# Optimization experiments

Measured on AMD Instinct MI355X. Metric: run time of the kernel, lower is better.

Reference implementation:

```python
import jax, jax.numpy as jnp
import numpy as np

N = 50000      # nodes
E = 800000     # edges (avg degree 16)
IN = 128       # input feature dim
H = 128        # hidden dim (all layers output H; out_channels unused in source)
DROP_P = 0.5


def setup_inputs() -> dict:
    key = jax.random.key(0)
    ks = jax.random.split(key, 8)
    s_in = 1.0 / np.sqrt(IN).astype(np.float32)
    s_h = 1.0 / np.sqrt(H).astype(np.float32)
    return {
        "x": jax.random.normal(ks[0], (N, IN), jnp.float32),
        "edge_index": jax.random.randint(ks[1], (2, E), 0, N, dtype=jnp.int32),
        "Wl0": jax.random.normal(ks[2], (H, IN), jnp.float32) * s_in,
        "bl0": jnp.zeros((H,), jnp.float32),
        "Wr0": jax.random.normal(ks[3], (H, IN), jnp.float32) * s_in,
        "Wl1": jax.random.normal(ks[4], (H, H), jnp.float32) * s_h,
        "bl1": jnp.zeros((H,), jnp.float32),
        "Wr1": jax.random.normal(ks[5], (H, H), jnp.float32) * s_h,
    }


def _sage_conv(x, src, dst, Wl, bl, Wr):
    # mean-aggregate neighbor messages: gather x[src], scatter-add to dst
    agg = jax.ops.segment_sum(x[src], dst, num_segments=N)          # [N, D]
    deg = jax.ops.segment_sum(jnp.ones((src.shape[0],), x.dtype), dst,
                              num_segments=N)                        # [N]
    agg = agg / jnp.maximum(deg, 1.0)[:, None]                       # scatter_mean (0 for isolated nodes)
    # PyG SAGEConv: lin_l(agg) (with bias) + lin_r(x) (no bias)
    return agg @ Wl.T + bl + x @ Wr.T


def reference(x, edge_index, Wl0, bl0, Wr0, Wl1, bl1, Wr1):
    src, dst = edge_index[0], edge_index[1]
    h = _sage_conv(x, src, dst, Wl0, bl0, Wr0)
    h = jax.nn.relu(h)
    # dropout(p=0.5, training=True) with a fixed key for determinism
    keep = jax.random.bernoulli(jax.random.key(42), 1.0 - DROP_P, h.shape)
    h = jnp.where(keep, h / (1.0 - DROP_P), 0.0)
    out = _sage_conv(h, src, dst, Wl1, bl1, Wr1)
    return out
```

## Files before the change

### kernel.cpp

```cpp
#include <hip/hip_runtime.h>
#include <hip/hip_bf16.h>


#define HDIM 128
#define KDIM 256
#define NBUK 256
#define BNODE 196
#define BCH 2048

typedef __attribute__((ext_vector_type(8))) short bshort8;
typedef __attribute__((ext_vector_type(4))) float f32x4;

__device__ __forceinline__ ushort f2b(float f) {
  __hip_bfloat16 h = __float2bfloat16(f);
  return *(ushort*)&h;
}
__device__ __forceinline__ float blo(unsigned int v) { return __uint_as_float(v << 16); }
__device__ __forceinline__ float bhi(unsigned int v) { return __uint_as_float(v & 0xffff0000u); }

__device__ __forceinline__ unsigned int tf_rotl(unsigned int x, int d) {
  return (x << d) | (x >> (32 - d));
}
__device__ __forceinline__ bool dropout_keep(unsigned int j) {
  unsigned int x0 = 0u, x1 = j;
  const unsigned int ks0 = 0u, ks1 = 42u, ks2 = 0x1BD11BDAu ^ 0u ^ 42u;
  x0 += ks0; x1 += ks1;
#define TF_R(r) { x0 += x1; x1 = tf_rotl(x1, (r)); x1 ^= x0; }
  TF_R(13) TF_R(15) TF_R(26) TF_R(6)
  x0 += ks1; x1 += ks2 + 1u;
  TF_R(17) TF_R(29) TF_R(16) TF_R(24)
  x0 += ks2; x1 += ks0 + 2u;
  TF_R(13) TF_R(15) TF_R(26) TF_R(6)
  x0 += ks0; x1 += ks1 + 3u;
  TF_R(17) TF_R(29) TF_R(16) TF_R(24)
  x0 += ks1; x1 += ks2 + 4u;
  TF_R(13) TF_R(15) TF_R(26) TF_R(6)
  x0 += ks2; x1 += ks0 + 5u;
#undef TF_R
  unsigned int r = x0 ^ x1;
  float u = __uint_as_float((r >> 9) | 0x3f800000u) - 1.0f;
  return u < 0.5f;
}

__global__ __launch_bounds__(256) void bhist_k(const int* __restrict__ dst,
                                               int* __restrict__ bucketCount, int E) {
  __shared__ int h[NBUK];
  h[threadIdx.x] = 0;
  __syncthreads();
  int begin = blockIdx.x * BCH;
  int n = min(BCH, E - begin);
  for (int i = threadIdx.x; i < n; i += 256) atomicAdd(&h[dst[begin + i] / BNODE], 1);
  __syncthreads();
  if (h[threadIdx.x]) atomicAdd(&bucketCount[threadIdx.x], h[threadIdx.x]);
}

__global__ __launch_bounds__(256) void bscan_k(const int* __restrict__ bucketCount,
                                               int* __restrict__ bucketStart,
                                               int* __restrict__ cursor) {
  __shared__ int tmp[NBUK];
  int v = bucketCount[threadIdx.x];
  tmp[threadIdx.x] = v;
  __syncthreads();
  for (int off = 1; off < NBUK; off <<= 1) {
    int t = (threadIdx.x >= off) ? tmp[threadIdx.x - off] : 0;
    __syncthreads();
    tmp[threadIdx.x] += t;
    __syncthreads();
  }
  int ex = tmp[threadIdx.x] - v;
  bucketStart[threadIdx.x] = ex;
  cursor[threadIdx.x] = ex;
}

__global__ __launch_bounds__(256) void bin_k(const int* __restrict__ src,
                                             const int* __restrict__ dst,
                                             int* __restrict__ cursor,
                                             unsigned int* __restrict__ pairs, int E) {
  __shared__ int hist[NBUK];
  __shared__ int lofs[NBUK];
  __shared__ int lcur[NBUK];
  __shared__ int gbase[NBUK];
  __shared__ unsigned int ordv[BCH];
  __shared__ unsigned char ordb[BCH];
  hist[threadIdx.x] = 0;
  __syncthreads();
  int begin = blockIdx.x * BCH;
  int n = min(BCH, E - begin);
  unsigned int vals[BCH / 256];
  int bks[BCH / 256];
  int cnt = 0;
  for (int i = threadIdx.x; i < n; i += 256) {
    int s = src[begin + i], d = dst[begin + i];
    int b = d / BNODE;
    int dloc = d - b * BNODE;
    vals[cnt] = ((unsigned int)s << 8) | (unsigned int)dloc;
    bks[cnt] = b;
    ++cnt;
    atomicAdd(&hist[b], 1);
  }
  __syncthreads();
  {
    int v = hist[threadIdx.x];
    lofs[threadIdx.x] = v;
    __syncthreads();
    for (int off = 1; off < NBUK; off <<= 1) {
      int t = (threadIdx.x >= off) ? lofs[threadIdx.x - off] : 0;
      __syncthreads();
      lofs[threadIdx.x] += t;
      __syncthreads();
    }
    int ex = lofs[threadIdx.x] - v;
    __syncthreads();
    lofs[threadIdx.x] = ex;
    lcur[threadIdx.x] = ex;
    gbase[threadIdx.x] = atomicAdd(&cursor[threadIdx.x], v);
  }
  __syncthreads();
  for (int k = 0; k < cnt; ++k) {
    int b = bks[k];
    int p = atomicAdd(&lcur[b], 1);
    ordv[p] = vals[k];
    ordb[p] = (unsigned char)b;
  }
  __syncthreads();
  for (int j = threadIdx.x; j < n; j += 256) {
    int b = ordb[j];
    pairs[gbase[b] + (j - lofs[b])] = ordv[j];
  }
}

__global__ __launch_bounds__(256) void build_k(const unsigned int* __restrict__ pairs,
                                               const int* __restrict__ bucketStart,
                                               const int* __restrict__ bucketCount,
                                               int* __restrict__ deg,
                                               int* __restrict__ rowptr,
                                               ushort* __restrict__ eidx, int N) {
  __shared__ int h[BNODE];
  __shared__ int lofs[BNODE];
  __shared__ int cur[BNODE];
  const int b = blockIdx.x;
  const int base = bucketStart[b];
  const int cnt = bucketCount[b];
  const int nodebase = b * BNODE;
  const int nloc = min(BNODE, N - nodebase);
  if (threadIdx.x < BNODE) h[threadIdx.x] = 0;
  __syncthreads();
  for (int i = threadIdx.x; i < cnt; i += 256) atomicAdd(&h[pairs[base + i] & 255u], 1);
  __syncthreads();
  if (threadIdx.x < BNODE) lofs[threadIdx.x] = h[threadIdx.x];
  __syncthreads();
  for (int off = 1; off < BNODE; off <<= 1) {
    int t = (threadIdx.x >= off && threadIdx.x < BNODE) ? lofs[threadIdx.x - off] : 0;
    __syncthreads();
    if (threadIdx.x < BNODE) lofs[threadIdx.x] += t;
    __syncthreads();
  }
  if (threadIdx.x < BNODE) {
    int ex = lofs[threadIdx.x] - h[threadIdx.x];
    cur[threadIdx.x] = ex;
    if (threadIdx.x < nloc) {
      deg[nodebase + threadIdx.x] = h[threadIdx.x];
      rowptr[nodebase + threadIdx.x] = base + ex;
    }
  }
  __syncthreads();
  for (int i = threadIdx.x; i < cnt; i += 256) {
    unsigned int v = pairs[base + i];
    int pos = atomicAdd(&cur[v & 255u], 1);
    eidx[base + pos] = (ushort)(v >> 8);
  }
}

__global__ __launch_bounds__(256) void cvt_x_k(const float* __restrict__ x,
                                               ushort* __restrict__ Ab, int N) {
  int t = blockIdx.x * 256 + threadIdx.x;
  if (t >= N * 32) return;
  int n = t >> 5, c4 = t & 31;
  float4 v = *(const float4*)&x[(size_t)n * HDIM + c4 * 4];
  uint2 p;
  p.x = (unsigned int)f2b(v.x) | ((unsigned int)f2b(v.y) << 16);
  p.y = (unsigned int)f2b(v.z) | ((unsigned int)f2b(v.w) << 16);
  *(uint2*)&Ab[(size_t)n * KDIM + HDIM + c4 * 4] = p;
}

__global__ __launch_bounds__(256) void cvt_w_k(const float* __restrict__ Wl0,
                                               const float* __restrict__ Wr0,
                                               const float* __restrict__ Wl1,
                                               const float* __restrict__ Wr1,
                                               ushort* __restrict__ Wc0,
                                               ushort* __restrict__ Wc1) {
  int t = blockIdx.x * 256 + threadIdx.x;
  int o = t >> 7, k = t & 127;
  Wc0[o * KDIM + k] = f2b(Wl0[t]);
  Wc0[o * KDIM + HDIM + k] = f2b(Wr0[t]);
  Wc1[o * KDIM + k] = f2b(Wl1[t]);
  Wc1[o * KDIM + HDIM + k] = f2b(Wr1[t]);
}

__global__ __launch_bounds__(256) void agg_b(const ushort* __restrict__ Xb,
                                             ushort* __restrict__ Ob,
                                             const ushort* __restrict__ eidx,
                                             const int* __restrict__ rowptr,
                                             const int* __restrict__ deg, int N) {
  const int lane = threadIdx.x & 63;
  const int n = blockIdx.x * 4 + (threadIdx.x >> 6);
  if (n >= N) return;
  const int start = rowptr[n];
  const int d = deg[n];
  const int co = 2 * lane;
  float a0 = 0.0f, a1 = 0.0f;
  int j = 0;
  for (; j + 4 <= d; j += 4) {
    int s0 = eidx[start + j + 0];
    int s1 = eidx[start + j + 1];
    int s2 = eidx[start + j + 2];
    int s3 = eidx[start + j + 3];
    unsigned int v0 = *(const unsigned int*)&Xb[(size_t)s0 * KDIM + HDIM + co];
    unsigned int v1 = *(const unsigned int*)&Xb[(size_t)s1 * KDIM + HDIM + co];
    unsigned int v2 = *(const unsigned int*)&Xb[(size_t)s2 * KDIM + HDIM + co];
    unsigned int v3 = *(const unsigned int*)&Xb[(size_t)s3 * KDIM + HDIM + co];
    a0 += blo(v0) + blo(v1) + blo(v2) + blo(v3);
    a1 += bhi(v0) + bhi(v1) + bhi(v2) + bhi(v3);
  }
  for (; j < d; ++j) {
    int s = eidx[start + j];
    unsigned int v = *(const unsigned int*)&Xb[(size_t)s * KDIM + HDIM + co];
    a0 += blo(v);
    a1 += bhi(v);
  }
  float rd = 1.0f / fmaxf((float)d, 1.0f);
  unsigned int p = (unsigned int)f2b(a0 * rd) | ((unsigned int)f2b(a1 * rd) << 16);
  *(unsigned int*)&Ob[(size_t)n * KDIM + co] = p;
}

template <int MODE>
__global__ __launch_bounds__(256) void gemm_mfma(const ushort* __restrict__ A,
                                                 const ushort* __restrict__ Wc,
                                                 ushort* __restrict__ hb,
                                                 float* __restrict__ fout,
                                                 const float* __restrict__ bias,
                                                 int N) {
  __shared__ char smem[67584];
  ushort* Wl = (ushort*)smem;
  float* Tl = (float*)smem;
  const int tid = threadIdx.x;
  const int lane = tid & 63;
  const int wid = tid >> 6;
  const int quad = lane >> 4;
  const int l15 = lane & 15;
  const int n0 = blockIdx.x * 64;

#pragma unroll
  for (int i = 0; i < 16; ++i) {
    int q = i * 256 + tid;
    int row = q >> 5, seg = q & 31;
    *(uint4*)&Wl[row * 264 + seg * 8] = *(const uint4*)&Wc[row * KDIM + seg * 8];
  }

  int rowA = n0 + wid * 16 + l15;
  if (rowA >= N) rowA = N - 1;
  bshort8 af[8];
#pragma unroll
  for (int ks = 0; ks < 8; ++ks)
    af[ks] = *(const bshort8*)&A[(size_t)rowA * KDIM + ks * 32 + quad * 8];

  f32x4 acc[8];
#pragma unroll
  for (int i = 0; i < 8; ++i) acc[i] = (f32x4){0.f, 0.f, 0.f, 0.f};

  __syncthreads();

#pragma unroll
  for (int ks = 0; ks < 8; ++ks) {
#pragma unroll
    for (int os = 0; os < 8; ++os) {
      bshort8 bf = *(const bshort8*)&Wl[(os * 16 + l15) * 264 + ks * 32 + quad * 8];
      acc[os] = __builtin_amdgcn_mfma_f32_16x16x32_bf16(af[ks], bf, acc[os], 0, 0, 0);
    }
  }

  __syncthreads();

  const int wbase = wid * (16 * 132);
#pragma unroll
  for (int os = 0; os < 8; ++os)
#pragma unroll
    for (int r = 0; r < 4; ++r)
      Tl[wbase + (quad * 4 + r) * 132 + os * 16 + l15] = acc[os][r];

  __syncthreads();

#pragma unroll
  for (int i = 0; i < 8; ++i) {
    int q = i * 64 + lane;
    int r = q >> 5;
    int c4 = q & 31;
    int n = n0 + wid * 16 + r;
    if (n >= N) continue;
    int c = c4 * 4;
    float4 v = *(float4*)&Tl[wbase + r * 132 + c];
    const float4 bv = *(const float4*)&bias[c];
    v.x += bv.x; v.y += bv.y; v.z += bv.z; v.w += bv.w;
    if (MODE == 1) {
      v.x = v.x > 0.0f ? v.x : 0.0f;
      v.y = v.y > 0.0f ? v.y : 0.0f;
      v.z = v.z > 0.0f ? v.z : 0.0f;
      v.w = v.w > 0.0f ? v.w : 0.0f;
      unsigned int fj = (unsigned int)n * HDIM + (unsigned int)c;
      v.x = dropout_keep(fj + 0u) ? v.x * 2.0f : 0.0f;
      v.y = dropout_keep(fj + 1u) ? v.y * 2.0f : 0.0f;
      v.z = dropout_keep(fj + 2u) ? v.z * 2.0f : 0.0f;
      v.w = dropout_keep(fj + 3u) ? v.w * 2.0f : 0.0f;
      uint2 p;
      p.x = (unsigned int)f2b(v.x) | ((unsigned int)f2b(v.y) << 16);
      p.y = (unsigned int)f2b(v.z) | ((unsigned int)f2b(v.w) << 16);
      *(uint2*)&hb[(size_t)n * KDIM + HDIM + c] = p;
    } else {
      *(float4*)&fout[(size_t)n * HDIM + c] = v;
    }
  }
}

extern "C" void kernel_launch(void* const* d_in, const int* in_sizes, int n_in,
                              void* d_out, int out_size, void* d_ws, size_t ws_size,
                              hipStream_t stream) {
  const float* x   = (const float*)d_in[0];
  const int*   ei  = (const int*)d_in[1];
  const float* Wl0 = (const float*)d_in[2];
  const float* bl0 = (const float*)d_in[3];
  const float* Wr0 = (const float*)d_in[4];
  const float* Wl1 = (const float*)d_in[5];
  const float* bl1 = (const float*)d_in[6];
  const float* Wr1 = (const float*)d_in[7];
  float* out = (float*)d_out;

  const int N = in_sizes[0] / HDIM;
  const int E = in_sizes[1] / 2;
  const int* src = ei;
  const int* dst = ei + E;

  const int Na = (N + 63) & ~63;
  int* bucketCount = (int*)d_ws;
  int* bucketStart = bucketCount + NBUK;
  int* cursor      = bucketStart + NBUK;
  int* deg         = cursor + NBUK;
  int* rowptr      = deg + Na;
  unsigned int* pairs = (unsigned int*)(rowptr + Na);
  ushort* eidx     = (ushort*)(pairs + E);
  size_t off = (((size_t)(eidx + E) - (size_t)d_ws) + 255) & ~(size_t)255;
  ushort* Wc0 = (ushort*)((char*)d_ws + off);
  ushort* Wc1 = Wc0 + 128 * KDIM;
  ushort* Ab  = Wc1 + 128 * KDIM;
  ushort* A2  = Ab + (size_t)N * KDIM;

  hipMemsetAsync(bucketCount, 0, NBUK * sizeof(int), stream);

  const int eb = (E + BCH - 1) / BCH;
  const int GB = (N + 63) / 64;
  const int AB = (N + 3) / 4;

  bhist_k<<<eb, 256, 0, stream>>>(dst, bucketCount, E);
  bscan_k<<<1, 256, 0, stream>>>(bucketCount, bucketStart, cursor);
  bin_k<<<eb, 256, 0, stream>>>(src, dst, cursor, pairs, E);
  build_k<<<NBUK, 256, 0, stream>>>(pairs, bucketStart, bucketCount, deg, rowptr, eidx, N);

  cvt_w_k<<<64, 256, 0, stream>>>(Wl0, Wr0, Wl1, Wr1, Wc0, Wc1);
  cvt_x_k<<<(N * 32 + 255) / 256, 256, 0, stream>>>(x, Ab, N);

  agg_b<<<AB, 256, 0, stream>>>(Ab, Ab, eidx, rowptr, deg, N);
  gemm_mfma<1><<<GB, 256, 0, stream>>>(Ab, Wc0, A2, nullptr, bl0, N);
  agg_b<<<AB, 256, 0, stream>>>(A2, A2, eidx, rowptr, deg, N);
  gemm_mfma<2><<<GB, 256, 0, stream>>>(A2, Wc1, nullptr, out, bl1, N);
}
```

Measured before the change: 241.8 us.

## Widen aggregation gathers to 16-byte loads and halve GEMM weight LDS footprint

The aggregation kernel now has each wavefront split into four 16-lane groups, each handling a different edge with 16-byte loads of 8 bf16 features, followed by a cross-group shuffle reduction. This replaces 4-byte per-lane gathers, so fewer, wider memory transactions are issued per edge row. The GEMM kernel now stages the weight matrix into LDS in two K-halves, cutting shared memory from about 66KB to 34KB to allow more resident blocks per CU. The cost is extra barriers and staging passes in the GEMM, plus shuffle reduction overhead and idle lanes on low-degree nodes in aggregation.

```diff
diff --git a/kernel.cpp b/kernel.cpp
--- a/kernel.cpp
+++ b/kernel.cpp
@@ -17,6 +17,9 @@
 }
 __device__ __forceinline__ float blo(unsigned int v) { return __uint_as_float(v << 16); }
 __device__ __forceinline__ float bhi(unsigned int v) { return __uint_as_float(v & 0xffff0000u); }
+__device__ __forceinline__ unsigned int pack2(float lo, float hi) {
+  return (unsigned int)f2b(lo) | ((unsigned int)f2b(hi) << 16);
+}
 
 __device__ __forceinline__ unsigned int tf_rotl(unsigned int x, int d) {
   return (x << d) | (x >> (32 - d));
@@ -178,8 +181,8 @@
   int n = t >> 5, c4 = t & 31;
   float4 v = *(const float4*)&x[(size_t)n * HDIM + c4 * 4];
   uint2 p;
-  p.x = (unsigned int)f2b(v.x) | ((unsigned int)f2b(v.y) << 16);
-  p.y = (unsigned int)f2b(v.z) | ((unsigned int)f2b(v.w) << 16);
+  p.x = pack2(v.x, v.y);
+  p.y = pack2(v.z, v.w);
   *(uint2*)&Ab[(size_t)n * KDIM + HDIM + c4 * 4] = p;
 }
 
@@ -207,30 +210,40 @@
   if (n >= N) return;
   const int start = rowptr[n];
   const int d = deg[n];
-  const int co = 2 * lane;
-  float a0 = 0.0f, a1 = 0.0f;
-  int j = 0;
-  for (; j + 4 <= d; j += 4) {
-    int s0 = eidx[start + j + 0];
-    int s1 = eidx[start + j + 1];
-    int s2 = eidx[start + j + 2];
-    int s3 = eidx[start + j + 3];
-    unsigned int v0 = *(const unsigned int*)&Xb[(size_t)s0 * KDIM + HDIM + co];
-    unsigned int v1 = *(const unsigned int*)&Xb[(size_t)s1 * KDIM + HDIM + co];
-    unsigned int v2 = *(const unsigned int*)&Xb[(size_t)s2 * KDIM + HDIM + co];
-    unsigned int v3 = *(const unsigned int*)&Xb[(size_t)s3 * KDIM + HDIM + co];
-    a0 += blo(v0) + blo(v1) + blo(v2) + blo(v3);
-    a1 += bhi(v0) + bhi(v1) + bhi(v2) + bhi(v3);
-  }
-  for (; j < d; ++j) {
-    int s = eidx[start + j];
-    unsigned int v = *(const unsigned int*)&Xb[(size_t)s * KDIM + HDIM + co];
-    a0 += blo(v);
-    a1 += bhi(v);
-  }
-  float rd = 1.0f / fmaxf((float)d, 1.0f);
-  unsigned int p = (unsigned int)f2b(a0 * rd) | ((unsigned int)f2b(a1 * rd) << 16);
-  *(unsigned int*)&Ob[(size_t)n * KDIM + co] = p;
+  const int g = lane >> 4;
+  const int cl = lane & 15;
+  float a0 = 0.f, a1 = 0.f, a2 = 0.f, a3 = 0.f, a4 = 0.f, a5 = 0.f, a6 = 0.f, a7 = 0.f;
+  for (int j = 0; j < d; j += 16) {
+#pragma unroll
+    for (int u = 0; u < 4; ++u) {
+      int e = j + u * 4 + g;
+      if (e < d) {
+        int s = eidx[start + e];
+        uint4 v = *(const uint4*)&Xb[(size_t)s * KDIM + HDIM + cl * 8];
+        a0 += blo(v.x); a1 += bhi(v.x);
+        a2 += blo(v.y); a3 += bhi(v.y);
+        a4 += blo(v.z); a5 += bhi(v.z);
+        a6 += blo(v.w); a7 += bhi(v.w);
+      }
+    }
+  }
+  a0 += __shfl_xor(a0, 16, 64); a0 += __shfl_xor(a0, 32, 64);
+  a1 += __shfl_xor(a1, 16, 64); a1 += __shfl_xor(a1, 32, 64);
+  a2 += __shfl_xor(a2, 16, 64); a2 += __shfl_xor(a2, 32, 64);
+  a3 += __shfl_xor(a3, 16, 64); a3 += __shfl_xor(a3, 32, 64);
+  a4 += __shfl_xor(a4, 16, 64); a4 += __shfl_xor(a4, 32, 64);
+  a5 += __shfl_xor(a5, 16, 64); a5 += __shfl_xor(a5, 32, 64);
+  a6 += __shfl_xor(a6, 16, 64); a6 += __shfl_xor(a6, 32, 64);
+  a7 += __shfl_xor(a7, 16, 64); a7 += __shfl_xor(a7, 32, 64);
+  if (g == 0) {
+    float rd = 1.0f / fmaxf((float)d, 1.0f);
+    uint4 p;
+    p.x = pack2(a0 * rd, a1 * rd);
+    p.y = pack2(a2 * rd, a3 * rd);
+    p.z = pack2(a4 * rd, a5 * rd);
+    p.w = pack2(a6 * rd, a7 * rd);
+    *(uint4*)&Ob[(size_t)n * KDIM + cl * 8] = p;
+  }
 }
 
 template <int MODE>
@@ -240,7 +253,7 @@
                                                  float* __restrict__ fout,
                                                  const float* __restrict__ bias,
                                                  int N) {
-  __shared__ char smem[67584];
+  __shared__ char smem[34816];
   ushort* Wl = (ushort*)smem;
   float* Tl = (float*)smem;
   const int tid = threadIdx.x;
@@ -250,13 +263,6 @@
   const int l15 = lane & 15;
   const int n0 = blockIdx.x * 64;
 
-#pragma unroll
-  for (int i = 0; i < 16; ++i) {
-    int q = i * 256 + tid;
-    int row = q >> 5, seg = q & 31;
-    *(uint4*)&Wl[row * 264 + seg * 8] = *(const uint4*)&Wc[row * KDIM + seg * 8];
-  }
-
   int rowA = n0 + wid * 16 + l15;
   if (rowA >= N) rowA = N - 1;
   bshort8 af[8];
@@ -268,14 +274,23 @@
 #pragma unroll
   for (int i = 0; i < 8; ++i) acc[i] = (f32x4){0.f, 0.f, 0.f, 0.f};
 
-  __syncthreads();
-
-#pragma unroll
-  for (int ks = 0; ks < 8; ++ks) {
-#pragma unroll
-    for (int os = 0; os < 8; ++os) {
-      bshort8 bf = *(const bshort8*)&Wl[(os * 16 + l15) * 264 + ks * 32 + quad * 8];
-      acc[os] = __builtin_amdgcn_mfma_f32_16x16x32_bf16(af[ks], bf, acc[os], 0, 0, 0);
+#pragma unroll
+  for (int half = 0; half < 2; ++half) {
+    __syncthreads();
+#pragma unroll
+    for (int i = 0; i < 8; ++i) {
+      int q = i * 256 + tid;
+      int row = q >> 4, seg = q & 15;
+      *(uint4*)&Wl[row * 136 + seg * 8] = *(const uint4*)&Wc[row * KDIM + half * HDIM + seg * 8];
+    }
+    __syncthreads();
+#pragma unroll
+    for (int ks = 0; ks < 4; ++ks) {
+#pragma unroll
+      for (int os = 0; os < 8; ++os) {
+        bshort8 bf = *(const bshort8*)&Wl[(os * 16 + l15) * 136 + ks * 32 + quad * 8];
+        acc[os] = __builtin_amdgcn_mfma_f32_16x16x32_bf16(af[half * 4 + ks], bf, acc[os], 0, 0, 0);
+      }
     }
   }
 
@@ -312,8 +327,8 @@
       v.z = dropout_keep(fj + 2u) ? v.z * 2.0f : 0.0f;
       v.w = dropout_keep(fj + 3u) ? v.w * 2.0f : 0.0f;
       uint2 p;
-      p.x = (unsigned int)f2b(v.x) | ((unsigned int)f2b(v.y) << 16);
-      p.y = (unsigned int)f2b(v.z) | ((unsigned int)f2b(v.w) << 16);
+      p.x = pack2(v.x, v.y);
+      p.y = pack2(v.z, v.w);
       *(uint2*)&hb[(size_t)n * KDIM + HDIM + c] = p;
     } else {
       *(float4*)&fout[(size_t)n * HDIM + c] = v;
```

Measured after the change: 238.4 us. Within noise of the previous version (-1.4%).
